# Performance work log

Hardware: AMD Instinct MI355X
Metric: run time of the kernel (lower is better)

## Reference

```python
import jax, jax.numpy as jnp
import numpy as np

B, L, D = 4, 2048, 1024
H = 16
HD = D // H  # head_dim = 64
BASE = 10000.0


def rope_cos_sin(seq_len, head_dim, dtype=jnp.float32):
    inv_freq = 1.0 / (BASE ** (jnp.arange(0, head_dim, 2, dtype=jnp.float32) / head_dim))
    t = jnp.arange(seq_len, dtype=jnp.float32)
    freqs = jnp.outer(t, inv_freq)  # [L, HD/2]
    return jnp.cos(freqs).astype(dtype), jnp.sin(freqs).astype(dtype)


def apply_rope(x, cos, sin):
    # x: [B, H, L, HD]; cos/sin: [L, HD/2]
    x1 = x[..., ::2]
    x2 = x[..., 1::2]
    c = cos[None, None, :, :]
    s = sin[None, None, :, :]
    # NOTE: original concatenates halves (does not re-interleave)
    return jnp.concatenate([x1 * c - x2 * s, x1 * s + x2 * c], axis=-1)


def setup_inputs() -> dict:
    key = jax.random.key(0)
    k1, k2, k3 = jax.random.split(key, 3)
    x = jax.random.normal(k1, (B, L, D), dtype=jnp.float32)
    W_qkv = jax.random.normal(k2, (3 * D, D), dtype=jnp.float32) * (D ** -0.5)
    W_proj = jax.random.normal(k3, (D, D), dtype=jnp.float32) * (D ** -0.5)
    return {"x": x, "W_qkv": W_qkv, "W_proj": W_proj}


def reference(x, W_qkv, W_proj):
    b, l, d = x.shape
    scale = HD ** -0.5
    qkv = jnp.einsum('bld,ed->ble', x, W_qkv)            # [B, L, 3D]
    qkv = qkv.reshape(b, l, 3, H, HD)
    q, k, v = (jnp.transpose(qkv[:, :, i], (0, 2, 1, 3)) for i in range(3))  # [B,H,L,HD]
    cos, sin = rope_cos_sin(l, HD, x.dtype)
    q = apply_rope(q, cos, sin)
    k = apply_rope(k, cos, sin)
    attn = jnp.einsum('bhqd,bhkd->bhqk', q, k) * scale   # [B,H,L,L]
    attn = jax.nn.softmax(attn, axis=-1)
    out = jnp.einsum('bhqk,bhkd->bhqd', attn, v)         # [B,H,L,HD]
    out = jnp.transpose(out, (0, 2, 1, 3)).reshape(b, l, d)
    return jnp.einsum('bld,ed->ble', out, W_proj)
```

## Files before the change

kernel.cpp:

```cpp
#include <hip/hip_runtime.h>
#include <hip/hip_bf16.h>

typedef unsigned short u16;
typedef unsigned int u32;
typedef __attribute__((ext_vector_type(8))) short bf16x8;
typedef __attribute__((ext_vector_type(4))) float f32x4;

#define NL 2048
#define NH 16

__device__ __forceinline__ float bf2f(u16 v) {
    union { float f; unsigned u; } x; x.u = ((unsigned)v) << 16; return x.f;
}
__device__ __forceinline__ u16 f2bf(float f) {
    union { __hip_bfloat16 h; u16 u; } x; x.h = __float2bfloat16(f); return x.u;
}
__device__ __forceinline__ u32 pk2(float a, float b) {
    union { float f; u32 u; } x, y; x.f = a; y.f = b;
    return ((x.u + 0x8000u) >> 16) | ((y.u + 0x8000u) & 0xffff0000u);
}
__device__ __forceinline__ u32 pkt(float lo, float hi) {
    union { float f; u32 u; } x, y; x.f = lo; y.f = hi;
    return __builtin_amdgcn_perm(y.u, x.u, 0x07060302u);
}
#if __has_builtin(__builtin_amdgcn_exp2f)
#define EXP2F(x) __builtin_amdgcn_exp2f(x)
#else
#define EXP2F(x) __expf((x) * 0.69314718056f)
#endif

__device__ __forceinline__ void gload_lds16(const u16* g, u16* l) {
    __builtin_amdgcn_global_load_lds(
        (__attribute__((address_space(1))) void*)(g),
        (__attribute__((address_space(3))) void*)(l), 16, 0, 0);
}

__global__ __launch_bounds__(256) void cast_all_k(const float* __restrict__ x,
                                                  const float* __restrict__ wq,
                                                  const float* __restrict__ wp,
                                                  u16* __restrict__ xo,
                                                  u16* __restrict__ wqo,
                                                  u16* __restrict__ wpo) {
    int i = blockIdx.x * 256 + threadIdx.x;
    const float* src; u16* dst; int off;
    if (i < 2097152)      { src = x;  dst = xo;  off = i; }
    else if (i < 2883584) { src = wq; dst = wqo; off = i - 2097152; }
    else                  { src = wp; dst = wpo; off = i - 2883584; }
    float4 v = *(const float4*)&src[(size_t)off * 4];
    u16 tmp[4] = {f2bf(v.x), f2bf(v.y), f2bf(v.z), f2bf(v.w)};
    *(ushort4*)&dst[(size_t)off * 4] = *(ushort4*)tmp;
}

__global__ __launch_bounds__(256) void rope_table_k(float* __restrict__ cosT,
                                                    float* __restrict__ sinT) {
    int idx = blockIdx.x * 256 + threadIdx.x;
    int l = idx >> 5, i = idx & 31;
    float invf = exp2f(-(float)i * 0.41524101186092029f);
    float ang = (float)l * invf;
    cosT[idx] = cosf(ang);
    sinT[idx] = sinf(ang);
}

template <typename OutT>
__global__ __launch_bounds__(256) void gemm_bt(const u16* __restrict__ A,
                                               const u16* __restrict__ Bm,
                                               OutT* __restrict__ C,
                                               int M, int N, int K) {
    __shared__ u16 As[128][64];
    __shared__ u16 Bs[128][64];
    const int t = threadIdx.x;
    const int lane = t & 63, wave = t >> 6;
    const int quad = lane >> 4, lrow = lane & 15;
    const int wr = wave >> 1, wc = wave & 1;
    const size_t m0 = (size_t)blockIdx.y * 128, n0 = (size_t)blockIdx.x * 128;

    const int srow = wave * 32 + (lane >> 3);
    const int scg  = (lane & 7) ^ (lane >> 3);

    f32x4 acc[4][4];
#pragma unroll
    for (int i = 0; i < 4; ++i)
#pragma unroll
        for (int j = 0; j < 4; ++j) acc[i][j] = (f32x4)0.0f;

    for (int k0 = 0; k0 < K; k0 += 64) {
#pragma unroll
        for (int j = 0; j < 4; ++j) {
            gload_lds16(&A[(m0 + srow + j * 8) * K + k0 + scg * 8],
                        &As[wave * 32 + j * 8][0]);
            gload_lds16(&Bm[(n0 + srow + j * 8) * K + k0 + scg * 8],
                        &Bs[wave * 32 + j * 8][0]);
        }
        __syncthreads();
#pragma unroll
        for (int ks = 0; ks < 2; ++ks) {
            bf16x8 av[4], bv[4];
#pragma unroll
            for (int i = 0; i < 4; ++i)
                av[i] = *(const bf16x8*)
                    &As[wr * 64 + i * 16 + lrow][(((ks << 2) | quad) ^ (lrow & 7)) << 3];
#pragma unroll
            for (int j = 0; j < 4; ++j)
                bv[j] = *(const bf16x8*)
                    &Bs[wc * 64 + j * 16 + lrow][(((ks << 2) | quad) ^ (lrow & 7)) << 3];
#pragma unroll
            for (int i = 0; i < 4; ++i)
#pragma unroll
                for (int j = 0; j < 4; ++j)
                    acc[i][j] = __builtin_amdgcn_mfma_f32_16x16x32_bf16(
                        av[i], bv[j], acc[i][j], 0, 0, 0);
        }
        __syncthreads();
    }
#pragma unroll
    for (int i = 0; i < 4; ++i)
#pragma unroll
        for (int r = 0; r < 4; ++r) {
            size_t row = m0 + wr * 64 + i * 16 + quad * 4 + r;
#pragma unroll
            for (int j = 0; j < 4; ++j) {
                size_t col = n0 + wc * 64 + j * 16 + lrow;
                if constexpr (sizeof(OutT) == 4)
                    C[row * N + col] = acc[i][j][r];
                else
                    C[row * N + col] = f2bf(acc[i][j][r]);
            }
        }
}

__global__ __launch_bounds__(256) void rope_vt_k(const u16* __restrict__ qkv,
                                                 const float* __restrict__ cosT,
                                                 const float* __restrict__ sinT,
                                                 u16* __restrict__ Q,
                                                 u16* __restrict__ Ko,
                                                 u16* __restrict__ VT) {
    __shared__ u16 vtile[64][72];
    const int lt = blockIdx.x, bh = blockIdx.y;
    const int b = bh >> 4, h = bh & 15;
    const int l0 = lt * 64;
    const int t = threadIdx.x;
    const float SC = 0.180336879f;
#pragma unroll
    for (int c = 0; c < 2; ++c) {
        int flat8 = c * 256 + t;
        int li = flat8 >> 3, dg = flat8 & 7;
        const u16* rowp = qkv + (size_t)(b * NL + l0 + li) * 3072 + h * 64 + dg * 8;
        uint4 qv = *(const uint4*)rowp;
        uint4 kv = *(const uint4*)(rowp + 1024);
        uint4 vv = *(const uint4*)(rowp + 2048);
        *(uint4*)&vtile[li][dg * 8] = vv;
        float4 cs = *(const float4*)&cosT[(l0 + li) * 32 + dg * 4];
        float4 sn = *(const float4*)&sinT[(l0 + li) * 32 + dg * 4];
        union { float f; u32 u; } w;
        float e0, o0, e1, o1, e2, o2, e3, o3;
        w.u = qv.x << 16; e0 = w.f; w.u = qv.x & 0xffff0000u; o0 = w.f;
        w.u = qv.y << 16; e1 = w.f; w.u = qv.y & 0xffff0000u; o1 = w.f;
        w.u = qv.z << 16; e2 = w.f; w.u = qv.z & 0xffff0000u; o2 = w.f;
        w.u = qv.w << 16; e3 = w.f; w.u = qv.w & 0xffff0000u; o3 = w.f;
        float c0 = cs.x * SC, c1 = cs.y * SC, c2 = cs.z * SC, c3 = cs.w * SC;
        float s0 = sn.x * SC, s1 = sn.y * SC, s2 = sn.z * SC, s3 = sn.w * SC;
        size_t ob = ((size_t)(b * NH + h) * NL + l0 + li) * 64;
        *(uint2*)&Q[ob + dg * 4] =
            make_uint2(pk2(e0 * c0 - o0 * s0, e1 * c1 - o1 * s1),
                       pk2(e2 * c2 - o2 * s2, e3 * c3 - o3 * s3));
        *(uint2*)&Q[ob + 32 + dg * 4] =
            make_uint2(pk2(e0 * s0 + o0 * c0, e1 * s1 + o1 * c1),
                       pk2(e2 * s2 + o2 * c2, e3 * s3 + o3 * c3));
        float f0, g0, f1, g1, f2, g2, f3, g3;
        w.u = kv.x << 16; f0 = w.f; w.u = kv.x & 0xffff0000u; g0 = w.f;
        w.u = kv.y << 16; f1 = w.f; w.u = kv.y & 0xffff0000u; g1 = w.f;
        w.u = kv.z << 16; f2 = w.f; w.u = kv.z & 0xffff0000u; g2 = w.f;
        w.u = kv.w << 16; f3 = w.f; w.u = kv.w & 0xffff0000u; g3 = w.f;
        *(uint2*)&Ko[ob + dg * 4] =
            make_uint2(pk2(f0 * cs.x - g0 * sn.x, f1 * cs.y - g1 * sn.y),
                       pk2(f2 * cs.z - g2 * sn.z, f3 * cs.w - g3 * sn.w));
        *(uint2*)&Ko[ob + 32 + dg * 4] =
            make_uint2(pk2(f0 * sn.x + g0 * cs.x, f1 * sn.y + g1 * cs.y),
                       pk2(f2 * sn.z + g2 * cs.z, f3 * sn.w + g3 * cs.w));
    }
    __syncthreads();
#pragma unroll
    for (int c = 0; c < 2; ++c) {
        int flat8 = c * 256 + t;
        int d = flat8 >> 3, lg = flat8 & 7;
        u16 tmp[8];
#pragma unroll
        for (int e = 0; e < 8; ++e) tmp[e] = vtile[lg * 8 + e][d];
        *(uint4*)&VT[((size_t)(bh * 64 + d)) * NL + l0 + lg * 8] = *(uint4*)tmp;
    }
}

__global__ __launch_bounds__(512, 4) void attn_k(const u16* __restrict__ Q,
                                                 const u16* __restrict__ Kg,
                                                 const u16* __restrict__ VT,
                                                 u16* __restrict__ Og) {
    __shared__ __align__(16) char smem[65536];
    u16 (*KsB)[64][64] = (u16(*)[64][64])(smem);
    u16 (*VsB)[64][64] = (u16(*)[64][64])(smem + 16384);
    u16* PsBase = (u16*)(smem + 32768);
    const int t = threadIdx.x;
    const int lane = t & 63, wave = t >> 6;
    const int quad = lane >> 4, lq = lane & 15;
    u16* PsW = PsBase + wave * 2048;

    const int qt = blockIdx.x, bh = blockIdx.y;
    const int q0 = qt * 256;
    const size_t qkbase = (size_t)bh * NL * 64;

    const int rsub = lane >> 3;
    const int scg  = (lane & 7) ^ rsub;

    u16 (*Qtmp)[64] = (u16(*)[64])(smem + 32768);
#pragma unroll
    for (int j = 0; j < 4; ++j)
        gload_lds16(&Q[qkbase + (size_t)(q0 + wave * 32 + j * 8 + rsub) * 64 + scg * 8],
                    &Qtmp[wave * 32 + j * 8][0]);
    const u16* kptr = Kg + qkbase + (size_t)(wave * 8 + rsub) * 64 + scg * 8;
    const u16* vptr = VT + qkbase + (size_t)(wave * 8 + rsub) * NL + scg * 8;
    gload_lds16(kptr, &KsB[0][wave * 8][0]);
    gload_lds16(vptr, &VsB[0][wave * 8][0]);
    kptr += 64 * 64;
    vptr += 64;
    __syncthreads();
    bf16x8 bq[2][2];
#pragma unroll
    for (int qh = 0; qh < 2; ++qh)
#pragma unroll
        for (int ks = 0; ks < 2; ++ks)
            bq[qh][ks] = *(const bf16x8*)
                &Qtmp[wave * 32 + qh * 16 + lq][(((ks << 2) | quad) ^ (lq & 7)) << 3];

    const bf16x8 ones = (bf16x8)(short)16256;
    f32x4 ot[2][4];
#pragma unroll
    for (int qh = 0; qh < 2; ++qh)
#pragma unroll
        for (int mt = 0; mt < 4; ++mt) ot[qh][mt] = (f32x4)0.0f;
    f32x4 lacc[2] = {(f32x4)0.0f, (f32x4)0.0f};

    for (int kc = 0; kc < NL / 64; ++kc) {
        __syncthreads();
        if (kc < NL / 64 - 1) {
            gload_lds16(kptr, &KsB[(kc + 1) & 1][wave * 8][0]);
            gload_lds16(vptr, &VsB[(kc + 1) & 1][wave * 8][0]);
            kptr += 64 * 64;
            vptr += 64;
        }
        const int cur = kc & 1;

        f32x4 st[2][4];
#pragma unroll
        for (int qh = 0; qh < 2; ++qh)
#pragma unroll
            for (int mt = 0; mt < 4; ++mt) st[qh][mt] = (f32x4)0.0f;
#pragma unroll
        for (int ks = 0; ks < 2; ++ks)
#pragma unroll
            for (int mt = 0; mt < 4; ++mt) {
                bf16x8 ak = *(const bf16x8*)
                    &KsB[cur][mt * 16 + lq][(((ks << 2) | quad) ^ (lq & 7)) << 3];
                st[0][mt] = __builtin_amdgcn_mfma_f32_16x16x32_bf16(ak, bq[0][ks], st[0][mt], 0, 0, 0);
                st[1][mt] = __builtin_amdgcn_mfma_f32_16x16x32_bf16(ak, bq[1][ks], st[1][mt], 0, 0, 0);
            }

#pragma unroll
        for (int qh = 0; qh < 2; ++qh)
#pragma unroll
            for (int mt = 0; mt < 4; ++mt) {
                int pblk = (mt * 2 + (quad >> 1)) ^ (lq & 7);
                *(uint2*)&PsW[(qh * 16 + lq) * 64 + pblk * 8 + (quad & 1) * 4] =
                    make_uint2(pkt(EXP2F(st[qh][mt][0]), EXP2F(st[qh][mt][1])),
                               pkt(EXP2F(st[qh][mt][2]), EXP2F(st[qh][mt][3])));
            }
        __builtin_amdgcn_s_waitcnt(0xc07f);

#pragma unroll
        for (int ks = 0; ks < 2; ++ks) {
            const int sw = (((ks << 2) | quad) ^ (lq & 7)) * 8;
            bf16x8 bp0 = *(const bf16x8*)&PsW[lq * 64 + sw];
            bf16x8 bp1 = *(const bf16x8*)&PsW[(16 + lq) * 64 + sw];
            lacc[0] = __builtin_amdgcn_mfma_f32_16x16x32_bf16(ones, bp0, lacc[0], 0, 0, 0);
            lacc[1] = __builtin_amdgcn_mfma_f32_16x16x32_bf16(ones, bp1, lacc[1], 0, 0, 0);
#pragma unroll
            for (int mt = 0; mt < 4; ++mt) {
                bf16x8 av = *(const bf16x8*)
                    &VsB[cur][mt * 16 + lq][(((ks << 2) | quad) ^ (lq & 7)) << 3];
                ot[0][mt] = __builtin_amdgcn_mfma_f32_16x16x32_bf16(av, bp0, ot[0][mt], 0, 0, 0);
                ot[1][mt] = __builtin_amdgcn_mfma_f32_16x16x32_bf16(av, bp1, ot[1][mt], 0, 0, 0);
            }
        }
    }

    __syncthreads();
    float* OT_ls = (float*)(smem + wave * 4352);
    float* Ls_ls = (float*)(smem + 34816);
    const int b = bh >> 4, h = bh & 15;
    const int qq = lane >> 2, dblk = lane & 3;
#pragma unroll
    for (int qh = 0; qh < 2; ++qh) {
#pragma unroll
        for (int mt = 0; mt < 4; ++mt)
#pragma unroll
            for (int r = 0; r < 4; ++r)
                OT_ls[(mt * 16 + quad * 4 + r) * 17 + lq] = ot[qh][mt][r];
        if (quad == 0) Ls_ls[wave * 16 + lq] = lacc[qh][0];
        __builtin_amdgcn_s_waitcnt(0xc07f);

        float rls = 1.0f / Ls_ls[wave * 16 + qq];
        u16 tmp[16];
#pragma unroll
        for (int e = 0; e < 16; ++e)
            tmp[e] = f2bf(OT_ls[(dblk * 16 + e) * 17 + qq] * rls);
        size_t orow = (size_t)b * NL + q0 + wave * 32 + qh * 16 + qq;
        size_t obase = orow * 1024 + h * 64 + dblk * 16;
        *(uint4*)&Og[obase] = *(uint4*)&tmp[0];
        *(uint4*)&Og[obase + 8] = *(uint4*)&tmp[8];
    }
}

extern "C" void kernel_launch(void* const* d_in, const int* in_sizes, int n_in,
                              void* d_out, int out_size, void* d_ws, size_t ws_size,
                              hipStream_t stream) {
    const float* x     = (const float*)d_in[0];
    const float* Wqkv  = (const float*)d_in[1];
    const float* Wproj = (const float*)d_in[2];
    float* out = (float*)d_out;

    char* ws = (char*)d_ws;
    u16* qkv     = (u16*)ws;
    u16* attnout = (u16*)ws;
    u16* Qw      = (u16*)(ws + 50331648);
    u16* Kw      = (u16*)(ws + 67108864);
    u16* VTw     = (u16*)(ws + 83886080);
    float* cosT  = (float*)(ws + 100663296);
    float* sinT  = (float*)(ws + 100925440);
    u16* x_bf    = (u16*)(ws + 101187584);
    u16* Wqkv_bf = (u16*)(ws + 117964800);
    u16* Wproj_bf= (u16*)(ws + 124256256);

    rope_table_k<<<256, 256, 0, stream>>>(cosT, sinT);
    cast_all_k<<<12288, 256, 0, stream>>>(x, Wqkv, Wproj, x_bf, Wqkv_bf, Wproj_bf);
    gemm_bt<u16><<<dim3(24, 64), 256, 0, stream>>>(x_bf, Wqkv_bf, qkv, 8192, 3072, 1024);
    rope_vt_k<<<dim3(32, 64), 256, 0, stream>>>(qkv, cosT, sinT, Qw, Kw, VTw);
    attn_k<<<dim3(8, 64), 512, 0, stream>>>(Qw, Kw, VTw, attnout);
    gemm_bt<float><<<dim3(8, 64), 256, 0, stream>>>(attnout, Wproj_bf, out, 8192, 1024, 1024);
}
```

Baseline: 266.5 us.

## Keep softmax probabilities in registers and use 4-wave blocks with 64 rows per wave

```diff
diff --git a/kernel.cpp b/kernel.cpp
--- a/kernel.cpp
+++ b/kernel.cpp
@@ -4,6 +4,7 @@
 typedef unsigned short u16;
 typedef unsigned int u32;
 typedef __attribute__((ext_vector_type(8))) short bf16x8;
+typedef __attribute__((ext_vector_type(4))) short bf16x4;
 typedef __attribute__((ext_vector_type(4))) float f32x4;
 
 #define NL 2048
@@ -190,67 +191,75 @@
     }
 }
 
-__global__ __launch_bounds__(512, 4) void attn_k(const u16* __restrict__ Q,
+__global__ __launch_bounds__(256, 2) void attn_k(const u16* __restrict__ Q,
                                                  const u16* __restrict__ Kg,
                                                  const u16* __restrict__ VT,
                                                  u16* __restrict__ Og) {
     __shared__ __align__(16) char smem[65536];
     u16 (*KsB)[64][64] = (u16(*)[64][64])(smem);
     u16 (*VsB)[64][64] = (u16(*)[64][64])(smem + 16384);
-    u16* PsBase = (u16*)(smem + 32768);
+    u16 (*Qtmp)[64]    = (u16(*)[64])(smem + 32768);
     const int t = threadIdx.x;
     const int lane = t & 63, wave = t >> 6;
     const int quad = lane >> 4, lq = lane & 15;
-    u16* PsW = PsBase + wave * 2048;
-
-    const int qt = blockIdx.x, bh = blockIdx.y;
+
+    const int flat = blockIdx.x;
+    const int bh = (flat & 7) | ((flat >> 6) << 3);
+    const int qt = (flat >> 3) & 7;
     const int q0 = qt * 256;
     const size_t qkbase = (size_t)bh * NL * 64;
 
     const int rsub = lane >> 3;
     const int scg  = (lane & 7) ^ rsub;
 
-    u16 (*Qtmp)[64] = (u16(*)[64])(smem + 32768);
-#pragma unroll
-    for (int j = 0; j < 4; ++j)
-        gload_lds16(&Q[qkbase + (size_t)(q0 + wave * 32 + j * 8 + rsub) * 64 + scg * 8],
-                    &Qtmp[wave * 32 + j * 8][0]);
-    const u16* kptr = Kg + qkbase + (size_t)(wave * 8 + rsub) * 64 + scg * 8;
-    const u16* vptr = VT + qkbase + (size_t)(wave * 8 + rsub) * NL + scg * 8;
-    gload_lds16(kptr, &KsB[0][wave * 8][0]);
-    gload_lds16(vptr, &VsB[0][wave * 8][0]);
+#pragma unroll
+    for (int j = 0; j < 8; ++j)
+        gload_lds16(&Q[qkbase + (size_t)(q0 + wave * 64 + j * 8 + rsub) * 64 + scg * 8],
+                    &Qtmp[wave * 64 + j * 8][0]);
+    const u16* kptr = Kg + qkbase + (size_t)(wave * 16 + rsub) * 64 + scg * 8;
+    const u16* vptr = VT + qkbase + (size_t)(wave * 16 + rsub) * NL + scg * 8;
+#pragma unroll
+    for (int j = 0; j < 2; ++j) {
+        gload_lds16(kptr + (size_t)j * 8 * 64, &KsB[0][wave * 16 + j * 8][0]);
+        gload_lds16(vptr + (size_t)j * 8 * NL, &VsB[0][wave * 16 + j * 8][0]);
+    }
     kptr += 64 * 64;
     vptr += 64;
     __syncthreads();
-    bf16x8 bq[2][2];
-#pragma unroll
-    for (int qh = 0; qh < 2; ++qh)
+    bf16x8 bq[4][2];
+#pragma unroll
+    for (int qh = 0; qh < 4; ++qh)
 #pragma unroll
         for (int ks = 0; ks < 2; ++ks)
             bq[qh][ks] = *(const bf16x8*)
-                &Qtmp[wave * 32 + qh * 16 + lq][(((ks << 2) | quad) ^ (lq & 7)) << 3];
-
-    const bf16x8 ones = (bf16x8)(short)16256;
-    f32x4 ot[2][4];
-#pragma unroll
-    for (int qh = 0; qh < 2; ++qh)
-#pragma unroll
-        for (int mt = 0; mt < 4; ++mt) ot[qh][mt] = (f32x4)0.0f;
-    f32x4 lacc[2] = {(f32x4)0.0f, (f32x4)0.0f};
+                &Qtmp[wave * 64 + qh * 16 + lq][(((ks << 2) | quad) ^ (lq & 7)) << 3];
+
+    const bf16x4 ones4 = (bf16x4)(short)16256;
+    f32x4 ot[4][4];
+#pragma unroll
+    for (int qh = 0; qh < 4; ++qh)
+#pragma unroll
+        for (int dt = 0; dt < 4; ++dt) ot[qh][dt] = (f32x4)0.0f;
+    f32x4 lacc[4] = {(f32x4)0.0f, (f32x4)0.0f, (f32x4)0.0f, (f32x4)0.0f};
+
+    const int lq7 = lq & 7, qh1 = quad >> 1, ql = (quad & 1) * 4;
 
     for (int kc = 0; kc < NL / 64; ++kc) {
         __syncthreads();
         if (kc < NL / 64 - 1) {
-            gload_lds16(kptr, &KsB[(kc + 1) & 1][wave * 8][0]);
-            gload_lds16(vptr, &VsB[(kc + 1) & 1][wave * 8][0]);
+#pragma unroll
+            for (int j = 0; j < 2; ++j) {
+                gload_lds16(kptr + (size_t)j * 8 * 64, &KsB[(kc + 1) & 1][wave * 16 + j * 8][0]);
+                gload_lds16(vptr + (size_t)j * 8 * NL, &VsB[(kc + 1) & 1][wave * 16 + j * 8][0]);
+            }
             kptr += 64 * 64;
             vptr += 64;
         }
         const int cur = kc & 1;
 
-        f32x4 st[2][4];
-#pragma unroll
-        for (int qh = 0; qh < 2; ++qh)
+        f32x4 st[4][4];
+#pragma unroll
+        for (int qh = 0; qh < 4; ++qh)
 #pragma unroll
             for (int mt = 0; mt < 4; ++mt) st[qh][mt] = (f32x4)0.0f;
 #pragma unroll
@@ -258,64 +267,54 @@
 #pragma unroll
             for (int mt = 0; mt < 4; ++mt) {
                 bf16x8 ak = *(const bf16x8*)
-                    &KsB[cur][mt * 16 + lq][(((ks << 2) | quad) ^ (lq & 7)) << 3];
-                st[0][mt] = __builtin_amdgcn_mfma_f32_16x16x32_bf16(ak, bq[0][ks], st[0][mt], 0, 0, 0);
-                st[1][mt] = __builtin_amdgcn_mfma_f32_16x16x32_bf16(ak, bq[1][ks], st[1][mt], 0, 0, 0);
-            }
-
-#pragma unroll
-        for (int qh = 0; qh < 2; ++qh)
+                    &KsB[cur][mt * 16 + lq][(((ks << 2) | quad) ^ lq7) << 3];
+#pragma unroll
+                for (int qh = 0; qh < 4; ++qh)
+                    st[qh][mt] = __builtin_amdgcn_mfma_f32_16x16x32_bf16(
+                        ak, bq[qh][ks], st[qh][mt], 0, 0, 0);
+            }
+
+        bf16x4 pa[4][4];
+#pragma unroll
+        for (int qh = 0; qh < 4; ++qh)
 #pragma unroll
             for (int mt = 0; mt < 4; ++mt) {
-                int pblk = (mt * 2 + (quad >> 1)) ^ (lq & 7);
-                *(uint2*)&PsW[(qh * 16 + lq) * 64 + pblk * 8 + (quad & 1) * 4] =
-                    make_uint2(pkt(EXP2F(st[qh][mt][0]), EXP2F(st[qh][mt][1])),
-                               pkt(EXP2F(st[qh][mt][2]), EXP2F(st[qh][mt][3])));
-            }
-        __builtin_amdgcn_s_waitcnt(0xc07f);
-
-#pragma unroll
-        for (int ks = 0; ks < 2; ++ks) {
-            const int sw = (((ks << 2) | quad) ^ (lq & 7)) * 8;
-            bf16x8 bp0 = *(const bf16x8*)&PsW[lq * 64 + sw];
-            bf16x8 bp1 = *(const bf16x8*)&PsW[(16 + lq) * 64 + sw];
-            lacc[0] = __builtin_amdgcn_mfma_f32_16x16x32_bf16(ones, bp0, lacc[0], 0, 0, 0);
-            lacc[1] = __builtin_amdgcn_mfma_f32_16x16x32_bf16(ones, bp1, lacc[1], 0, 0, 0);
-#pragma unroll
-            for (int mt = 0; mt < 4; ++mt) {
-                bf16x8 av = *(const bf16x8*)
-                    &VsB[cur][mt * 16 + lq][(((ks << 2) | quad) ^ (lq & 7)) << 3];
-                ot[0][mt] = __builtin_amdgcn_mfma_f32_16x16x32_bf16(av, bp0, ot[0][mt], 0, 0, 0);
-                ot[1][mt] = __builtin_amdgcn_mfma_f32_16x16x32_bf16(av, bp1, ot[1][mt], 0, 0, 0);
-            }
-        }
-    }
-
-    __syncthreads();
-    float* OT_ls = (float*)(smem + wave * 4352);
-    float* Ls_ls = (float*)(smem + 34816);
+                union { uint2 u; bf16x4 v; } c;
+                c.u = make_uint2(pkt(EXP2F(st[qh][mt][0]), EXP2F(st[qh][mt][1])),
+                                 pkt(EXP2F(st[qh][mt][2]), EXP2F(st[qh][mt][3])));
+                pa[qh][mt] = c.v;
+            }
+
+#pragma unroll
+        for (int mt = 0; mt < 4; ++mt) {
+#pragma unroll
+            for (int qh = 0; qh < 4; ++qh)
+                lacc[qh] = __builtin_amdgcn_mfma_f32_16x16x16bf16_1k(
+                    pa[qh][mt], ones4, lacc[qh], 0, 0, 0);
+            const int voff = ((mt * 2 + qh1) ^ lq7) * 8 + ql;
+#pragma unroll
+            for (int dt = 0; dt < 4; ++dt) {
+                bf16x4 bv = *(const bf16x4*)&VsB[cur][dt * 16 + lq][voff];
+#pragma unroll
+                for (int qh = 0; qh < 4; ++qh)
+                    ot[qh][dt] = __builtin_amdgcn_mfma_f32_16x16x16bf16_1k(
+                        pa[qh][mt], bv, ot[qh][dt], 0, 0, 0);
+            }
+        }
+    }
+
     const int b = bh >> 4, h = bh & 15;
-    const int qq = lane >> 2, dblk = lane & 3;
-#pragma unroll
-    for (int qh = 0; qh < 2; ++qh) {
-#pragma unroll
-        for (int mt = 0; mt < 4; ++mt)
-#pragma unroll
-            for (int r = 0; r < 4; ++r)
-                OT_ls[(mt * 16 + quad * 4 + r) * 17 + lq] = ot[qh][mt][r];
-        if (quad == 0) Ls_ls[wave * 16 + lq] = lacc[qh][0];
-        __builtin_amdgcn_s_waitcnt(0xc07f);
-
-        float rls = 1.0f / Ls_ls[wave * 16 + qq];
-        u16 tmp[16];
-#pragma unroll
-        for (int e = 0; e < 16; ++e)
-            tmp[e] = f2bf(OT_ls[(dblk * 16 + e) * 17 + qq] * rls);
-        size_t orow = (size_t)b * NL + q0 + wave * 32 + qh * 16 + qq;
-        size_t obase = orow * 1024 + h * 64 + dblk * 16;
-        *(uint4*)&Og[obase] = *(uint4*)&tmp[0];
-        *(uint4*)&Og[obase + 8] = *(uint4*)&tmp[8];
-    }
+#pragma unroll
+    for (int qh = 0; qh < 4; ++qh)
+#pragma unroll
+        for (int r = 0; r < 4; ++r) {
+            float rls = 1.0f / lacc[qh][r];
+            size_t row = (size_t)b * NL + q0 + wave * 64 + qh * 16 + quad * 4 + r;
+            size_t obase = row * 1024 + h * 64 + lq;
+#pragma unroll
+            for (int dt = 0; dt < 4; ++dt)
+                Og[obase + dt * 16] = f2bf(ot[qh][dt][r] * rls);
+        }
 }
 
 extern "C" void kernel_launch(void* const* d_in, const int* in_sizes, int n_in,
@@ -342,6 +341,6 @@
     cast_all_k<<<12288, 256, 0, stream>>>(x, Wqkv, Wproj, x_bf, Wqkv_bf, Wproj_bf);
     gemm_bt<u16><<<dim3(24, 64), 256, 0, stream>>>(x_bf, Wqkv_bf, qkv, 8192, 3072, 1024);
     rope_vt_k<<<dim3(32, 64), 256, 0, stream>>>(qkv, cosT, sinT, Qw, Kw, VTw);
-    attn_k<<<dim3(8, 64), 512, 0, stream>>>(Qw, Kw, VTw, attnout);
+    attn_k<<<dim3(512), 256, 0, stream>>>(Qw, Kw, VTw, attnout);
     gemm_bt<float><<<dim3(8, 64), 256, 0, stream>>>(attnout, Wproj_bf, out, 8192, 1024, 1024);
 }
```

After: 277.7 us. 4.2% more time.
